# Kernel tuning notes

Measured on AMD Instinct MI355X. Metric: run time of the kernel, lower is better.

Reference implementation:

```python
import jax, jax.numpy as jnp
import numpy as np

N_HEADS = 8
HEAD_C = 48
NC = N_HEADS * HEAD_C  # 384
N_GROUPS = 4
GC = NC // N_GROUPS  # 96
STRIDE = 2
EPS = 1e-5


def conv1x1(x, w, b):
    # x: (B,C,H,W), w: (O,C), b: (O,)
    return jnp.einsum('bchw,oc->bohw', x, w) + b[None, :, None, None]


def ref_points(Hk, Wk, dtype):
    ry = jnp.linspace(0.5, Hk - 0.5, Hk, dtype=dtype) / (Hk - 1.0) * 2.0 - 1.0
    rx = jnp.linspace(0.5, Wk - 0.5, Wk, dtype=dtype) / (Wk - 1.0) * 2.0 - 1.0
    return jnp.stack(jnp.meshgrid(ry, rx, indexing='ij'), axis=-1)  # (Hk,Wk,2) in (y,x)


def grid_sample_bilinear(img, grid):
    # img: (N,C,H,W); grid: (N,Hg,Wg,2) xy in [-1,1]; align_corners=True, zeros padding
    N, C, H, W = img.shape
    gx = (grid[..., 0] + 1.0) * 0.5 * (W - 1)
    gy = (grid[..., 1] + 1.0) * 0.5 * (H - 1)
    x0 = jnp.floor(gx); y0 = jnp.floor(gy)
    x1 = x0 + 1.0;      y1 = y0 + 1.0
    wx1 = gx - x0; wx0 = 1.0 - wx1
    wy1 = gy - y0; wy0 = 1.0 - wy1

    def gather(ix, iy):
        valid = (ix >= 0) & (ix <= W - 1) & (iy >= 0) & (iy <= H - 1)
        ixc = jnp.clip(ix, 0, W - 1).astype(jnp.int32)
        iyc = jnp.clip(iy, 0, H - 1).astype(jnp.int32)
        vals = jax.vmap(lambda im, yy, xx: im[:, yy, xx])(img, iyc, ixc)  # (N,C,Hg,Wg)
        return vals * valid[:, None].astype(img.dtype)

    v00 = gather(x0, y0); v01 = gather(x1, y0)
    v10 = gather(x0, y1); v11 = gather(x1, y1)
    return (v00 * (wx0 * wy0)[:, None] + v01 * (wx1 * wy0)[:, None]
            + v10 * (wx0 * wy1)[:, None] + v11 * (wx1 * wy1)[:, None])


def _forward(x, Wq, bq, Wk, bk, Wv, bv, Wo, bo,
             off_dw_w, off_dw_b, ln_g, ln_b, off_pw_w):
    B, C, H, W = x.shape
    q = conv1x1(x, Wq, bq)                               # (B,C,H,W)
    q_off = q.reshape(B * N_GROUPS, GC, H, W)
    # offset net: depthwise 3x3 stride-2 conv -> channel LN -> GELU -> 1x1 to 2 ch
    h = jax.lax.conv_general_dilated(
        q_off, off_dw_w, (STRIDE, STRIDE), ((1, 1), (1, 1)),
        dimension_numbers=('NCHW', 'OIHW', 'NCHW'), feature_group_count=GC)
    h = h + off_dw_b[None, :, None, None]
    mu = h.mean(axis=1, keepdims=True)
    var = ((h - mu) ** 2).mean(axis=1, keepdims=True)
    h = (h - mu) / jnp.sqrt(var + EPS) * ln_g[None, :, None, None] + ln_b[None, :, None, None]
    h = jax.nn.gelu(h, approximate=False)
    offset = jnp.einsum('bchw,oc->bohw', h, off_pw_w)    # (B*g, 2, Hk, Wk), ch0=y, ch1=x
    Hk, Wk_ = offset.shape[2], offset.shape[3]
    rng = jnp.array([1.0 / (Hk - 1.0), 1.0 / (Wk_ - 1.0)], x.dtype).reshape(1, 2, 1, 1)
    offset = jnp.tanh(offset) * rng                      # offset_range_factor = 1
    offset = offset.transpose(0, 2, 3, 1)                # (B*g, Hk, Wk, 2) yx
    ref = ref_points(Hk, Wk_, x.dtype)                   # (Hk, Wk, 2) yx
    pos = offset + ref[None]
    xs = grid_sample_bilinear(x.reshape(B * N_GROUPS, GC, H, W), pos[..., ::-1])
    n = Hk * Wk_
    xs = xs.reshape(B, C, 1, n)
    k = conv1x1(xs, Wk, bk).reshape(B * N_HEADS, HEAD_C, n)
    v = conv1x1(xs, Wv, bv).reshape(B * N_HEADS, HEAD_C, n)
    qh = q.reshape(B * N_HEADS, HEAD_C, H * W)
    attn = jnp.einsum('bcm,bcn->bmn', qh, k) * (HEAD_C ** -0.5)
    attn = jax.nn.softmax(attn, axis=2)
    out = jnp.einsum('bmn,bcn->bcm', attn, v).reshape(B, C, H, W)
    y = conv1x1(out, Wo, bo)
    ref_b = jnp.broadcast_to(ref[None, None], (B, N_GROUPS, Hk, Wk_, 2))
    return y, pos.reshape(B, N_GROUPS, Hk, Wk_, 2), ref_b


def setup_inputs() -> dict:
    key = jax.random.key(0)
    ks = jax.random.split(key, 12)
    s = 0.02
    return {
        'x': jax.random.normal(ks[0], (8, NC, 56, 56), jnp.float32),
        'Wq': jax.random.normal(ks[1], (NC, NC), jnp.float32) * s,
        'bq': jnp.zeros((NC,), jnp.float32),
        'Wk': jax.random.normal(ks[2], (NC, NC), jnp.float32) * s,
        'bk': jnp.zeros((NC,), jnp.float32),
        'Wv': jax.random.normal(ks[3], (NC, NC), jnp.float32) * s,
        'bv': jnp.zeros((NC,), jnp.float32),
        'Wo': jax.random.normal(ks[4], (NC, NC), jnp.float32) * s,
        'bo': jnp.zeros((NC,), jnp.float32),
        'off_dw_w': jax.random.normal(ks[5], (GC, 1, 3, 3), jnp.float32) * 0.1,
        'off_dw_b': jnp.zeros((GC,), jnp.float32),
        'ln_g': jnp.ones((GC,), jnp.float32),
        'ln_b': jnp.zeros((GC,), jnp.float32),
        'off_pw_w': jax.random.normal(ks[6], (2, GC), jnp.float32) * 0.1,
    }


def reference(x, Wq, bq, Wk, bk, Wv, bv, Wo, bo,
              off_dw_w, off_dw_b, ln_g, ln_b, off_pw_w):
    return _forward(x, Wq, bq, Wk, bk, Wv, bv, Wo, bo,
                    off_dw_w, off_dw_b, ln_g, ln_b, off_pw_w)
```

## Files before the change

kernel.cpp:

```cpp
#include <hip/hip_runtime.h>
#include <math.h>

constexpr int BATCH = 8;
constexpr int NC    = 384;
constexpr int H     = 56, W = 56, HW = 3136;
constexpr int NPTS  = 784;
constexpr int NG    = 4, GC = 96;
constexpr int NH    = 8, HC = 48;

typedef __attribute__((ext_vector_type(8))) short short8;
typedef __attribute__((ext_vector_type(4))) float f32x4;
typedef __attribute__((ext_vector_type(4))) unsigned short us4;

__device__ inline unsigned short f2bf(float f) {
    union { float f; unsigned u; } v; v.f = f;
    unsigned r = v.u + 0x7FFF + ((v.u >> 16) & 1);
    return (unsigned short)(r >> 16);
}
__device__ inline unsigned short f2bf_t(float f) {
    union { float f; unsigned u; } v; v.f = f;
    return (unsigned short)(v.u >> 16);
}
__device__ inline float bf2f(unsigned short u) {
    union { unsigned u; float f; } v; v.u = (unsigned)u << 16;
    return v.f;
}
__device__ inline float wred_sum(float v) {
    #pragma unroll
    for (int off = 32; off > 0; off >>= 1) v += __shfl_xor(v, off);
    return v;
}

__global__ __launch_bounds__(256) void transpose_cvt(
    const float* __restrict__ x, unsigned short* __restrict__ xT)
{
    __shared__ unsigned short Ls[64 * 68];
    int b = blockIdx.z, c0 = blockIdx.y * 64, hw0 = blockIdx.x * 64;
    const float* xb = x + ((size_t)b * NC + c0) * HW + hw0;
    int t = threadIdx.x;
    #pragma unroll
    for (int i = 0; i < 4; i++) {
        int u = t + i * 256;
        int cc = u >> 4, f4 = (u & 15) * 4;
        float4 v = *(const float4*)&xb[(size_t)cc * HW + f4];
        us4 p; p[0] = f2bf(v.x); p[1] = f2bf(v.y); p[2] = f2bf(v.z); p[3] = f2bf(v.w);
        *(us4*)&Ls[cc * 68 + f4] = p;
    }
    __syncthreads();
    unsigned short* xTb = xT + ((size_t)b * HW + hw0) * NC + c0;
    #pragma unroll
    for (int i = 0; i < 4; i++) {
        int u = t + i * 256;
        int hw = u >> 4, cg = (u & 15) * 4;
        us4 p;
        p[0] = Ls[(cg + 0) * 68 + hw];
        p[1] = Ls[(cg + 1) * 68 + hw];
        p[2] = Ls[(cg + 2) * 68 + hw];
        p[3] = Ls[(cg + 3) * 68 + hw];
        *(us4*)&xTb[(size_t)hw * NC + cg] = p;
    }
}

__global__ __launch_bounds__(256) void wcvt(
    const float* __restrict__ w0, const float* __restrict__ w1,
    const float* __restrict__ w2, const float* __restrict__ w3,
    unsigned short* __restrict__ o0, unsigned short* __restrict__ o1,
    unsigned short* __restrict__ o2, unsigned short* __restrict__ o3)
{
    const float* src; unsigned short* dst;
    switch (blockIdx.y) {
        case 0: src = w0; dst = o0; break;
        case 1: src = w1; dst = o1; break;
        case 2: src = w2; dst = o2; break;
        default: src = w3; dst = o3; break;
    }
    int idx = (blockIdx.x * 256 + threadIdx.x) * 4;
    float4 v = *(const float4*)&src[idx];
    us4 p; p[0] = f2bf(v.x); p[1] = f2bf(v.y); p[2] = f2bf(v.z); p[3] = f2bf(v.w);
    *(us4*)&dst[idx] = p;
}

template<int MODE>
__global__ __launch_bounds__(256) void gemm_bf16(
    const unsigned short* __restrict__ A, const float* __restrict__ bias,
    const unsigned short* __restrict__ BT,
    float* __restrict__ Cf, unsigned short* __restrict__ Cb, int N)
{
    int b  = blockIdx.z;
    int n0 = blockIdx.x * 128;
    int m0 = blockIdx.y * 128;
    const unsigned short* BTb = BT + (size_t)b * N * NC;

    __shared__ unsigned short As[128 * 40];
    __shared__ unsigned short Bs[128 * 40];

    int t = threadIdx.x;
    int wave = t >> 6, lane = t & 63;
    int quad = lane >> 4, col = lane & 15;
    int wm = (wave >> 1) * 64, wn = (wave & 1) * 64;

    const short8 z8 = {0,0,0,0,0,0,0,0};
    f32x4 acc[4][4];
    #pragma unroll
    for (int i = 0; i < 4; i++)
        #pragma unroll
        for (int j = 0; j < 4; j++) acc[i][j] = (f32x4){0.f, 0.f, 0.f, 0.f};

    for (int k0 = 0; k0 < NC; k0 += 32) {
        #pragma unroll
        for (int i = 0; i < 2; i++) {
            int u = t + i * 256;
            int mm = u >> 2, kc = (u & 3) * 8;
            *(short8*)&As[mm * 40 + kc] =
                *(const short8*)&A[(size_t)(m0 + mm) * NC + k0 + kc];
        }
        #pragma unroll
        for (int i = 0; i < 2; i++) {
            int u = t + i * 256;
            int nn = u >> 2, kc = (u & 3) * 8;
            short8 val = z8;
            if (n0 + nn < N)
                val = *(const short8*)&BTb[(size_t)(n0 + nn) * NC + k0 + kc];
            *(short8*)&Bs[nn * 40 + kc] = val;
        }
        __syncthreads();

        short8 af[4], bf[4];
        #pragma unroll
        for (int mt = 0; mt < 4; mt++)
            af[mt] = *(const short8*)&As[(wm + mt * 16 + col) * 40 + quad * 8];
        #pragma unroll
        for (int nt = 0; nt < 4; nt++)
            bf[nt] = *(const short8*)&Bs[(wn + nt * 16 + col) * 40 + quad * 8];
        #pragma unroll
        for (int mt = 0; mt < 4; mt++)
            #pragma unroll
            for (int nt = 0; nt < 4; nt++)
                acc[mt][nt] = __builtin_amdgcn_mfma_f32_16x16x32_bf16(
                    af[mt], bf[nt], acc[mt][nt], 0, 0, 0);
        __syncthreads();
    }

    if constexpr (MODE == 0) {
        float* Cfb = Cf + (size_t)b * NC * N;
        #pragma unroll
        for (int mt = 0; mt < 4; mt++) {
            #pragma unroll
            for (int r = 0; r < 4; r++) {
                int m = m0 + wm + mt * 16 + quad * 4 + r;
                float bv = bias[m];
                #pragma unroll
                for (int nt = 0; nt < 4; nt++) {
                    int n = n0 + wn + nt * 16 + col;
                    if (n < N) Cfb[(size_t)m * N + n] = acc[mt][nt][r] + bv;
                }
            }
        }
    } else if constexpr (MODE == 2) {
        unsigned short* Kb = Cb + (size_t)b * N * NC;
        #pragma unroll
        for (int mt = 0; mt < 4; mt++) {
            int mb = m0 + wm + mt * 16 + quad * 4;
            float bv[4];
            #pragma unroll
            for (int r = 0; r < 4; r++) bv[r] = bias[mb + r];
            #pragma unroll
            for (int nt = 0; nt < 4; nt++) {
                int n = n0 + wn + nt * 16 + col;
                if (n < N) {
                    us4 p;
                    #pragma unroll
                    for (int r = 0; r < 4; r++) p[r] = f2bf(acc[mt][nt][r] + bv[r]);
                    *(us4*)&Kb[(size_t)n * NC + mb] = p;
                }
            }
        }
    } else {
        unsigned short* Vb = Cb + (size_t)b * NC * N;
        #pragma unroll
        for (int mt = 0; mt < 4; mt++) {
            #pragma unroll
            for (int r = 0; r < 4; r++) {
                int m = m0 + wm + mt * 16 + quad * 4 + r;
                float bv = bias[m];
                #pragma unroll
                for (int nt = 0; nt < 4; nt++) {
                    int n = n0 + wn + nt * 16 + col;
                    if (n < N) Vb[(size_t)m * N + n] = f2bf(acc[mt][nt][r] + bv);
                }
            }
        }
    }
}

__global__ __launch_bounds__(256) void offset_kernel(
    const unsigned short* __restrict__ qT, const float* __restrict__ dww,
    const float* __restrict__ dwb, const float* __restrict__ lng,
    const float* __restrict__ lnb, const float* __restrict__ pww,
    float* __restrict__ pos_out,   float* __restrict__ ref_out)
{
    int wave = threadIdx.x >> 6, l = threadIdx.x & 63;
    int bg = blockIdx.y, b = bg >> 2, g = bg & 3;
    int s  = blockIdx.x * 4 + wave;
    int py = s / 28, px = s - py * 28;
    bool has2 = l < 32;
    int c0 = l, c1 = 64 + l;

    const unsigned short* qb = qT + (size_t)b * HW * NC + g * GC;

    float h0 = 0.f, h1 = 0.f;
    #pragma unroll
    for (int ky = 0; ky < 3; ky++) {
        int yy = py * 2 - 1 + ky;
        if (yy < 0 || yy >= H) continue;
        #pragma unroll
        for (int kx = 0; kx < 3; kx++) {
            int xx = px * 2 - 1 + kx;
            if (xx < 0 || xx >= W) continue;
            const unsigned short* row = qb + (size_t)(yy * W + xx) * NC;
            float w0 = dww[c0 * 9 + ky * 3 + kx];
            h0 = fmaf(bf2f(row[c0]), w0, h0);
            if (has2) {
                float w1 = dww[c1 * 9 + ky * 3 + kx];
                h1 = fmaf(bf2f(row[c1]), w1, h1);
            }
        }
    }
    h0 += dwb[c0];
    if (has2) h1 += dwb[c1];

    float mu = wred_sum(h0 + (has2 ? h1 : 0.f)) * (1.f / GC);
    float d0 = h0 - mu, d1 = h1 - mu;
    float var = wred_sum(d0 * d0 + (has2 ? d1 * d1 : 0.f)) * (1.f / GC);
    float rstd = rsqrtf(var + 1e-5f);

    float hn0 = d0 * rstd * lng[c0] + lnb[c0];
    float ge0 = 0.5f * hn0 * (1.f + erff(hn0 * 0.70710678118654752f));
    float ge1 = 0.f;
    if (has2) {
        float hn1 = d1 * rstd * lng[c1] + lnb[c1];
        ge1 = 0.5f * hn1 * (1.f + erff(hn1 * 0.70710678118654752f));
    }

    float offy = wred_sum(ge0 * pww[c0] + (has2 ? ge1 * pww[c1] : 0.f));
    float offx = wred_sum(ge0 * pww[GC + c0] + (has2 ? ge1 * pww[GC + c1] : 0.f));

    if (l == 0) {
        float ry = (2.f * py + 1.f) / 27.f - 1.f;
        float rx = (2.f * px + 1.f) / 27.f - 1.f;
        size_t idx = ((size_t)bg * NPTS + s) * 2;
        pos_out[idx]     = tanhf(offy) * (1.f / 27.f) + ry;
        pos_out[idx + 1] = tanhf(offx) * (1.f / 27.f) + rx;
        ref_out[idx]     = ry;
        ref_out[idx + 1] = rx;
    }
}

__global__ __launch_bounds__(256) void sample_kernel(
    const float* __restrict__ x, const float* __restrict__ pos,
    unsigned short* __restrict__ xsT)
{
    int bg = blockIdx.y;
    int b  = bg >> 2, g = bg & 3;
    int s  = blockIdx.x * 8 + (threadIdx.x >> 5);
    int l  = threadIdx.x & 31;

    const float* pg = pos + ((size_t)bg * NPTS + s) * 2;
    float py = pg[0], px = pg[1];
    float gx = (px + 1.f) * 27.5f;
    float gy = (py + 1.f) * 27.5f;
    float x0f = floorf(gx), y0f = floorf(gy);
    int ix0 = (int)x0f, iy0 = (int)y0f;
    int ix1 = ix0 + 1,  iy1 = iy0 + 1;
    float wx1 = gx - x0f, wx0 = 1.f - wx1;
    float wy1 = gy - y0f, wy0 = 1.f - wy1;
    bool vx0 = (ix0 >= 0) && (ix0 < W);
    bool vx1 = (ix1 >= 0) && (ix1 < W);
    bool vy0 = (iy0 >= 0) && (iy0 < H);
    bool vy1 = (iy1 >= 0) && (iy1 < H);
    int cx0 = vx0 ? ix0 : 0, cx1 = vx1 ? ix1 : 0;
    int cy0 = vy0 ? iy0 : 0, cy1 = vy1 ? iy1 : 0;
    float w00 = (vx0 && vy0) ? wx0 * wy0 : 0.f;
    float w01 = (vx1 && vy0) ? wx1 * wy0 : 0.f;
    float w10 = (vx0 && vy1) ? wx0 * wy1 : 0.f;
    float w11 = (vx1 && vy1) ? wx1 * wy1 : 0.f;
    int i00 = cy0 * W + cx0, i01 = cy0 * W + cx1;
    int i10 = cy1 * W + cx0, i11 = cy1 * W + cx1;

    const float* xb = x + ((size_t)b * NC + g * GC) * HW;
    unsigned short* orow = xsT + ((size_t)b * NPTS + s) * NC + g * GC;
    #pragma unroll
    for (int ci = 0; ci < 3; ci++) {
        int c = l + ci * 32;
        const float* xc = xb + (size_t)c * HW;
        float val = xc[i00] * w00 + xc[i01] * w01 + xc[i10] * w10 + xc[i11] * w11;
        orow[c] = f2bf(val);
    }
}

#define KS_STRIDE 56
#define VS_STRIDE 136
#define PS_STRIDE 40

__device__ inline short8 scale8(short8 v, float s) {
    short8 r;
    #pragma unroll
    for (int j = 0; j < 8; j++)
        r[j] = (short)f2bf(bf2f((unsigned short)v[j]) * s);
    return r;
}

__global__ __launch_bounds__(256) void attn_mfma(
    const unsigned short* __restrict__ qT, const unsigned short* __restrict__ kt,
    const unsigned short* __restrict__ vt, unsigned short* __restrict__ aoT)
{
    __shared__ __align__(16) unsigned short smem[18816];
    unsigned short* Ks = smem;
    unsigned short* Vs = Ks + 128 * KS_STRIDE;
    unsigned short* Ps = Vs + 48 * VS_STRIDE;

    int t    = threadIdx.x;
    int wave = t >> 6, lane = t & 63;
    int quad = lane >> 4, col = lane & 15;

    int bh = blockIdx.y;
    int b  = bh >> 3, h = bh & 7;
    int m0 = blockIdx.x * 128;
    const unsigned short* KT = kt + (size_t)b * NPTS * NC + h * HC;
    const unsigned short* VT = vt + ((size_t)b * NC + h * HC) * NPTS;

    const float scale = 0.14433756729740643f;
    const short8 z8 = {0,0,0,0,0,0,0,0};

    int gm0 = m0 + wave * 32 + col;
    int gm1 = gm0 + 16;
    short8 qb0[2], qb1[2];
    {
        int cg0 = gm0 < HW ? gm0 : HW - 1;
        int cg1 = gm1 < HW ? gm1 : HW - 1;
        const unsigned short* r0 = qT + ((size_t)b * HW + cg0) * NC + h * HC;
        const unsigned short* r1 = qT + ((size_t)b * HW + cg1) * NC + h * HC;
        qb0[0] = scale8(*(const short8*)&r0[quad * 8], scale);
        qb0[1] = scale8(*(const short8*)&r1[quad * 8], scale);
        if (quad < 2) {
            qb1[0] = scale8(*(const short8*)&r0[32 + quad * 8], scale);
            qb1[1] = scale8(*(const short8*)&r1[32 + quad * 8], scale);
        } else { qb1[0] = z8; qb1[1] = z8; }
    }

    unsigned short* pane0 = Ps + (wave * 2 + 0) * 16 * PS_STRIDE;
    unsigned short* pane1 = Ps + (wave * 2 + 1) * 16 * PS_STRIDE;

    float l_acc[2] = {0.f, 0.f};
    f32x4 acc_o[2][3];
    #pragma unroll
    for (int s2 = 0; s2 < 2; s2++)
        #pragma unroll
        for (int ct = 0; ct < 3; ct++) acc_o[s2][ct] = (f32x4){0.f, 0.f, 0.f, 0.f};

    for (int ci = 0; ci < 7; ci++) {
        int k0 = ci * 128;

        {
            int key = t >> 1;
            int pbase = (t & 1) * 3;
            const unsigned short* krow = KT + (size_t)(k0 + key) * NC + pbase * 8;
            bool kv = (k0 + key) < NPTS;
            #pragma unroll
            for (int i = 0; i < 3; i++) {
                short8 val = kv ? *(const short8*)(krow + i * 8) : z8;
                *(short8*)&Ks[key * KS_STRIDE + (pbase + i) * 8] = val;
            }
        }
        #pragma unroll
        for (int i = 0; i < 3; i++) {
            int li = t + i * 256;
            int chan = li >> 4, part = li & 15;
            short8 val = (k0 + part * 8 < NPTS)
                ? *(const short8*)&VT[(size_t)chan * NPTS + k0 + part * 8] : z8;
            *(short8*)&Vs[chan * VS_STRIDE + part * 8] = val;
        }
        __syncthreads();

        #pragma unroll
        for (int s2 = 0; s2 < 4; s2++) {
            #pragma unroll
            for (int jth = 0; jth < 2; jth++) {
                int jt = s2 * 2 + jth;
                int keyl = jt * 16 + col;
                short8 kb0 = *(const short8*)&Ks[keyl * KS_STRIDE + quad * 8];
                short8 kb1 = (quad < 2)
                    ? *(const short8*)&Ks[keyl * KS_STRIDE + 32 + quad * 8] : z8;
                bool valid = (k0 + jt * 16) < NPTS;
                #pragma unroll
                for (int set = 0; set < 2; set++) {
                    f32x4 sa = {0.f, 0.f, 0.f, 0.f};
                    sa = __builtin_amdgcn_mfma_f32_16x16x32_bf16(kb0, qb0[set], sa, 0, 0, 0);
                    sa = __builtin_amdgcn_mfma_f32_16x16x32_bf16(kb1, qb1[set], sa, 0, 0, 0);
                    us4 p = {0, 0, 0, 0};
                    if (valid) {
                        #pragma unroll
                        for (int r = 0; r < 4; r++) {
                            float pv = __expf(sa[r]);
                            l_acc[set] += pv;
                            p[r] = f2bf_t(pv);
                        }
                    }
                    unsigned short* pane = set ? pane1 : pane0;
                    *(us4*)&pane[col * PS_STRIDE + jth * 16 + quad * 4] = p;
                }
            }
            short8 pb0 = *(const short8*)&pane0[col * PS_STRIDE + quad * 8];
            short8 pb1 = *(const short8*)&pane1[col * PS_STRIDE + quad * 8];
            #pragma unroll
            for (int ct = 0; ct < 3; ct++) {
                short8 va = *(const short8*)&Vs[(ct * 16 + col) * VS_STRIDE + s2 * 32 + quad * 8];
                acc_o[0][ct] = __builtin_amdgcn_mfma_f32_16x16x32_bf16(va, pb0, acc_o[0][ct], 0, 0, 0);
                acc_o[1][ct] = __builtin_amdgcn_mfma_f32_16x16x32_bf16(va, pb1, acc_o[1][ct], 0, 0, 0);
            }
        }
        __syncthreads();
    }

    #pragma unroll
    for (int set = 0; set < 2; set++) {
        float l = l_acc[set];
        l += __shfl_xor(l, 16);
        l += __shfl_xor(l, 32);
        float inv = 1.f / l;
        int gm = set ? gm1 : gm0;
        if (gm < HW) {
            unsigned short* orow = aoT + ((size_t)b * HW + gm) * NC + h * HC;
            #pragma unroll
            for (int ct = 0; ct < 3; ct++) {
                us4 p;
                #pragma unroll
                for (int r = 0; r < 4; r++) p[r] = f2bf(acc_o[set][ct][r] * inv);
                *(us4*)&orow[ct * 16 + quad * 4] = p;
            }
        }
    }
}

extern "C" void kernel_launch(void* const* d_in, const int* in_sizes, int n_in,
                              void* d_out, int out_size, void* d_ws, size_t ws_size,
                              hipStream_t stream)
{
    const float* x   = (const float*)d_in[0];
    const float* Wq  = (const float*)d_in[1];
    const float* bq  = (const float*)d_in[2];
    const float* Wk  = (const float*)d_in[3];
    const float* bk  = (const float*)d_in[4];
    const float* Wv  = (const float*)d_in[5];
    const float* bv  = (const float*)d_in[6];
    const float* Wo  = (const float*)d_in[7];
    const float* bo  = (const float*)d_in[8];
    const float* dww = (const float*)d_in[9];
    const float* dwb = (const float*)d_in[10];
    const float* lng = (const float*)d_in[11];
    const float* lnb = (const float*)d_in[12];
    const float* pww = (const float*)d_in[13];

    float* out     = (float*)d_out;
    float* y_out   = out;
    float* pos_out = out + (size_t)BATCH * NC * HW;
    float* ref_out = pos_out + (size_t)BATCH * NG * NPTS * 2;

    const size_t NBIG = (size_t)BATCH * NC * HW;
    const size_t NSML = (size_t)BATCH * NC * NPTS;

    unsigned short* xT   = (unsigned short*)d_ws;
    unsigned short* qT   = xT   + NBIG;
    unsigned short* xsT  = qT   + NBIG;
    unsigned short* kt_w = xsT  + NSML;
    unsigned short* vt_w = kt_w + NSML;
    unsigned short* aoT  = vt_w + NSML;
    unsigned short* wqb  = aoT  + NBIG;
    unsigned short* wkb  = wqb + NC * NC;
    unsigned short* wvb  = wkb + NC * NC;
    unsigned short* wob  = wvb + NC * NC;

    transpose_cvt<<<dim3(49, 6, BATCH), 256, 0, stream>>>(x, xT);
    wcvt<<<dim3(144, 4), 256, 0, stream>>>(Wq, Wk, Wv, Wo, wqb, wkb, wvb, wob);
    gemm_bf16<2><<<dim3(25, 3, BATCH), 256, 0, stream>>>(wqb, bq, xT, nullptr, qT, HW);
    offset_kernel<<<dim3(196, BATCH * NG), 256, 0, stream>>>(
        qT, dww, dwb, lng, lnb, pww, pos_out, ref_out);
    sample_kernel<<<dim3(98, BATCH * NG), 256, 0, stream>>>(x, pos_out, xsT);
    gemm_bf16<2><<<dim3(7, 3, BATCH), 256, 0, stream>>>(wkb, bk, xsT, nullptr, kt_w, NPTS);
    gemm_bf16<3><<<dim3(7, 3, BATCH), 256, 0, stream>>>(wvb, bv, xsT, nullptr, vt_w, NPTS);
    attn_mfma<<<dim3((HW + 127) / 128, BATCH * NH), 256, 0, stream>>>(qT, kt_w, vt_w, aoT);
    gemm_bf16<0><<<dim3(25, 3, BATCH), 256, 0, stream>>>(wob, bo, aoT, y_out, nullptr, HW);
}
```

Baseline: 330.4 us.

## Fuse K/V projections, sample from bf16 xT, read K/V directly in attention

```diff
diff --git a/kernel.cpp b/kernel.cpp
--- a/kernel.cpp
+++ b/kernel.cpp
@@ -64,14 +64,14 @@
 __global__ __launch_bounds__(256) void wcvt(
     const float* __restrict__ w0, const float* __restrict__ w1,
     const float* __restrict__ w2, const float* __restrict__ w3,
-    unsigned short* __restrict__ o0, unsigned short* __restrict__ o1,
-    unsigned short* __restrict__ o2, unsigned short* __restrict__ o3)
+    unsigned short* __restrict__ o0, unsigned short* __restrict__ okv,
+    unsigned short* __restrict__ o3)
 {
     const float* src; unsigned short* dst;
     switch (blockIdx.y) {
         case 0: src = w0; dst = o0; break;
-        case 1: src = w1; dst = o1; break;
-        case 2: src = w2; dst = o2; break;
+        case 1: src = w1; dst = okv; break;
+        case 2: src = w2; dst = okv + NC * NC; break;
         default: src = w3; dst = o3; break;
     }
     int idx = (blockIdx.x * 256 + threadIdx.x) * 4;
@@ -83,8 +83,9 @@
 template<int MODE>
 __global__ __launch_bounds__(256) void gemm_bf16(
     const unsigned short* __restrict__ A, const float* __restrict__ bias,
-    const unsigned short* __restrict__ BT,
-    float* __restrict__ Cf, unsigned short* __restrict__ Cb, int N)
+    const float* __restrict__ bias2, const unsigned short* __restrict__ BT,
+    float* __restrict__ Cf, unsigned short* __restrict__ Cb,
+    unsigned short* __restrict__ Cb2, int N)
 {
     int b  = blockIdx.z;
     int n0 = blockIdx.x * 128;
@@ -176,17 +177,38 @@
             }
         }
     } else {
-        unsigned short* Vb = Cb + (size_t)b * NC * N;
-        #pragma unroll
-        for (int mt = 0; mt < 4; mt++) {
-            #pragma unroll
-            for (int r = 0; r < 4; r++) {
-                int m = m0 + wm + mt * 16 + quad * 4 + r;
-                float bv = bias[m];
+        if (m0 < NC) {
+            unsigned short* Kb = Cb + (size_t)b * N * NC;
+            #pragma unroll
+            for (int mt = 0; mt < 4; mt++) {
+                int mb = m0 + wm + mt * 16 + quad * 4;
+                float bv[4];
+                #pragma unroll
+                for (int r = 0; r < 4; r++) bv[r] = bias[mb + r];
                 #pragma unroll
                 for (int nt = 0; nt < 4; nt++) {
                     int n = n0 + wn + nt * 16 + col;
-                    if (n < N) Vb[(size_t)m * N + n] = f2bf(acc[mt][nt][r] + bv);
+                    if (n < N) {
+                        us4 p;
+                        #pragma unroll
+                        for (int r = 0; r < 4; r++) p[r] = f2bf(acc[mt][nt][r] + bv[r]);
+                        *(us4*)&Kb[(size_t)n * NC + mb] = p;
+                    }
+                }
+            }
+        } else {
+            unsigned short* Vb = Cb2 + (size_t)b * NC * N;
+            #pragma unroll
+            for (int mt = 0; mt < 4; mt++) {
+                #pragma unroll
+                for (int r = 0; r < 4; r++) {
+                    int m = m0 - NC + wm + mt * 16 + quad * 4 + r;
+                    float bv = bias2[m];
+                    #pragma unroll
+                    for (int nt = 0; nt < 4; nt++) {
+                        int n = n0 + wn + nt * 16 + col;
+                        if (n < N) Vb[(size_t)m * N + n] = f2bf(acc[mt][nt][r] + bv);
+                    }
                 }
             }
         }
@@ -257,7 +279,7 @@
 }
 
 __global__ __launch_bounds__(256) void sample_kernel(
-    const float* __restrict__ x, const float* __restrict__ pos,
+    const unsigned short* __restrict__ xT, const float* __restrict__ pos,
     unsigned short* __restrict__ xsT)
 {
     int bg = blockIdx.y;
@@ -284,22 +306,22 @@
     float w01 = (vx1 && vy0) ? wx1 * wy0 : 0.f;
     float w10 = (vx0 && vy1) ? wx0 * wy1 : 0.f;
     float w11 = (vx1 && vy1) ? wx1 * wy1 : 0.f;
-    int i00 = cy0 * W + cx0, i01 = cy0 * W + cx1;
-    int i10 = cy1 * W + cx0, i11 = cy1 * W + cx1;
-
-    const float* xb = x + ((size_t)b * NC + g * GC) * HW;
+
+    const unsigned short* xb = xT + (size_t)b * HW * NC + g * GC;
+    const unsigned short* r00 = xb + (size_t)(cy0 * W + cx0) * NC;
+    const unsigned short* r01 = xb + (size_t)(cy0 * W + cx1) * NC;
+    const unsigned short* r10 = xb + (size_t)(cy1 * W + cx0) * NC;
+    const unsigned short* r11 = xb + (size_t)(cy1 * W + cx1) * NC;
     unsigned short* orow = xsT + ((size_t)b * NPTS + s) * NC + g * GC;
     #pragma unroll
     for (int ci = 0; ci < 3; ci++) {
         int c = l + ci * 32;
-        const float* xc = xb + (size_t)c * HW;
-        float val = xc[i00] * w00 + xc[i01] * w01 + xc[i10] * w10 + xc[i11] * w11;
+        float val = bf2f(r00[c]) * w00 + bf2f(r01[c]) * w01
+                  + bf2f(r10[c]) * w10 + bf2f(r11[c]) * w11;
         orow[c] = f2bf(val);
     }
 }
 
-#define KS_STRIDE 56
-#define VS_STRIDE 136
 #define PS_STRIDE 40
 
 __device__ inline short8 scale8(short8 v, float s) {
@@ -314,10 +336,7 @@
     const unsigned short* __restrict__ qT, const unsigned short* __restrict__ kt,
     const unsigned short* __restrict__ vt, unsigned short* __restrict__ aoT)
 {
-    __shared__ __align__(16) unsigned short smem[18816];
-    unsigned short* Ks = smem;
-    unsigned short* Vs = Ks + 128 * KS_STRIDE;
-    unsigned short* Ps = Vs + 48 * VS_STRIDE;
+    __shared__ __align__(16) unsigned short Ps[8 * 16 * PS_STRIDE];
 
     int t    = threadIdx.x;
     int wave = t >> 6, lane = t & 63;
@@ -361,36 +380,16 @@
     for (int ci = 0; ci < 7; ci++) {
         int k0 = ci * 128;
 
-        {
-            int key = t >> 1;
-            int pbase = (t & 1) * 3;
-            const unsigned short* krow = KT + (size_t)(k0 + key) * NC + pbase * 8;
-            bool kv = (k0 + key) < NPTS;
-            #pragma unroll
-            for (int i = 0; i < 3; i++) {
-                short8 val = kv ? *(const short8*)(krow + i * 8) : z8;
-                *(short8*)&Ks[key * KS_STRIDE + (pbase + i) * 8] = val;
-            }
-        }
-        #pragma unroll
-        for (int i = 0; i < 3; i++) {
-            int li = t + i * 256;
-            int chan = li >> 4, part = li & 15;
-            short8 val = (k0 + part * 8 < NPTS)
-                ? *(const short8*)&VT[(size_t)chan * NPTS + k0 + part * 8] : z8;
-            *(short8*)&Vs[chan * VS_STRIDE + part * 8] = val;
-        }
-        __syncthreads();
-
         #pragma unroll
         for (int s2 = 0; s2 < 4; s2++) {
             #pragma unroll
             for (int jth = 0; jth < 2; jth++) {
                 int jt = s2 * 2 + jth;
-                int keyl = jt * 16 + col;
-                short8 kb0 = *(const short8*)&Ks[keyl * KS_STRIDE + quad * 8];
-                short8 kb1 = (quad < 2)
-                    ? *(const short8*)&Ks[keyl * KS_STRIDE + 32 + quad * 8] : z8;
+                int key = k0 + jt * 16 + col;
+                key = key < NPTS ? key : NPTS - 1;
+                const unsigned short* krow = KT + (size_t)key * NC;
+                short8 kb0 = *(const short8*)&krow[quad * 8];
+                short8 kb1 = (quad < 2) ? *(const short8*)&krow[32 + quad * 8] : z8;
                 bool valid = (k0 + jt * 16) < NPTS;
                 #pragma unroll
                 for (int set = 0; set < 2; set++) {
@@ -412,14 +411,15 @@
             }
             short8 pb0 = *(const short8*)&pane0[col * PS_STRIDE + quad * 8];
             short8 pb1 = *(const short8*)&pane1[col * PS_STRIDE + quad * 8];
+            int voff = k0 + s2 * 32 + quad * 8;
+            voff = voff <= (NPTS - 8) ? voff : (NPTS - 8);
             #pragma unroll
             for (int ct = 0; ct < 3; ct++) {
-                short8 va = *(const short8*)&Vs[(ct * 16 + col) * VS_STRIDE + s2 * 32 + quad * 8];
+                short8 va = *(const short8*)&VT[(size_t)(ct * 16 + col) * NPTS + voff];
                 acc_o[0][ct] = __builtin_amdgcn_mfma_f32_16x16x32_bf16(va, pb0, acc_o[0][ct], 0, 0, 0);
                 acc_o[1][ct] = __builtin_amdgcn_mfma_f32_16x16x32_bf16(va, pb1, acc_o[1][ct], 0, 0, 0);
             }
         }
-        __syncthreads();
     }
 
     #pragma unroll
@@ -476,18 +476,20 @@
     unsigned short* vt_w = kt_w + NSML;
     unsigned short* aoT  = vt_w + NSML;
     unsigned short* wqb  = aoT  + NBIG;
-    unsigned short* wkb  = wqb + NC * NC;
-    unsigned short* wvb  = wkb + NC * NC;
-    unsigned short* wob  = wvb + NC * NC;
+    unsigned short* wob  = wqb + NC * NC;
+    unsigned short* wkv  = wob + NC * NC;
 
     transpose_cvt<<<dim3(49, 6, BATCH), 256, 0, stream>>>(x, xT);
-    wcvt<<<dim3(144, 4), 256, 0, stream>>>(Wq, Wk, Wv, Wo, wqb, wkb, wvb, wob);
-    gemm_bf16<2><<<dim3(25, 3, BATCH), 256, 0, stream>>>(wqb, bq, xT, nullptr, qT, HW);
+    wcvt<<<dim3(144, 4), 256, 0, stream>>>(Wq, Wk, Wv, Wo, wqb, wkv, wob);
+    gemm_bf16<2><<<dim3(25, 3, BATCH), 256, 0, stream>>>(
+        wqb, bq, nullptr, xT, nullptr, qT, nullptr, HW);
     offset_kernel<<<dim3(196, BATCH * NG), 256, 0, stream>>>(
         qT, dww, dwb, lng, lnb, pww, pos_out, ref_out);
-    sample_kernel<<<dim3(98, BATCH * NG), 256, 0, stream>>>(x, pos_out, xsT);
-    gemm_bf16<2><<<dim3(7, 3, BATCH), 256, 0, stream>>>(wkb, bk, xsT, nullptr, kt_w, NPTS);
-    gemm_bf16<3><<<dim3(7, 3, BATCH), 256, 0, stream>>>(wvb, bv, xsT, nullptr, vt_w, NPTS);
-    attn_mfma<<<dim3((HW + 127) / 128, BATCH * NH), 256, 0, stream>>>(qT, kt_w, vt_w, aoT);
-    gemm_bf16<0><<<dim3(25, 3, BATCH), 256, 0, stream>>>(wob, bo, aoT, y_out, nullptr, HW);
-}
+    sample_kernel<<<dim3(98, BATCH * NG), 256, 0, stream>>>(xT, pos_out, xsT);
+    gemm_bf16<4><<<dim3(7, 6, BATCH), 256, 0, stream>>>(
+        wkv, bk, bv, xsT, nullptr, kt_w, vt_w, NPTS);
+    attn_mfma<<<dim3((HW + 127) / 128, BATCH * NH), 256, 0, stream>>>(
+        qT, kt_w, vt_w, aoT);
+    gemm_bf16<0><<<dim3(25, 3, BATCH), 256, 0, stream>>>(
+        wob, bo, nullptr, aoT, y_out, nullptr, nullptr, HW);
+}
```

After: 331.2 us. No clear change (+0.3%).
